# Kernel optimization log

Hardware: AMD Instinct MI355X
Metric: run time of the kernel (lower is better)

## Reference

```python
import jax, jax.numpy as jnp
import numpy as np

N = 100000          # number of active sparse points
GRID = 800          # coordinate grid extent (2D)
KS = 9              # 3x3 kernel offsets
C_IN = 24
C_HID = 144         # round(24 * 6)
C_OUT = 24
EPS = 1e-5


def _build_kernel_map():
    """Build MinkowskiEngine-style kernel map for a 3x3 stride-1 channelwise conv.
    Returns (in_idx, out_idx, off_id), each [KS*N] int32. Invalid (no neighbor)
    entries point to sentinel row N so the padded gather/scatter is a no-op."""
    rng = np.random.default_rng(0)
    flat = rng.choice(GRID * GRID, size=N, replace=False)  # unique 2D coords
    ys, xs = flat // GRID, flat % GRID
    coord_to_idx = -np.ones(GRID * GRID, dtype=np.int64)
    coord_to_idx[flat] = np.arange(N)
    in_chunks, out_chunks, off_chunks = [], [], []
    pts = np.arange(N, dtype=np.int64)
    k = 0
    for dy in (-1, 0, 1):
        for dx in (-1, 0, 1):
            ny, nx = ys + dy, xs + dx
            inside = (ny >= 0) & (ny < GRID) & (nx >= 0) & (nx < GRID)
            nflat = np.clip(ny, 0, GRID - 1) * GRID + np.clip(nx, 0, GRID - 1)
            nidx = np.where(inside, coord_to_idx[nflat], -1)
            valid = nidx >= 0
            in_chunks.append(np.where(valid, nidx, N))
            out_chunks.append(np.where(valid, pts, N))
            off_chunks.append(np.full(N, k, dtype=np.int64))
            k += 1
    in_idx = np.concatenate(in_chunks).astype(np.int32)
    out_idx = np.concatenate(out_chunks).astype(np.int32)
    off_id = np.concatenate(off_chunks).astype(np.int32)
    return in_idx, out_idx, off_id


def setup_inputs() -> dict:
    key = jax.random.key(0)
    ks = jax.random.split(key, 4)
    in_idx, out_idx, off_id = _build_kernel_map()
    return {
        "feats": jax.random.normal(ks[0], (N, C_IN), jnp.float32),
        "w1": jax.random.normal(ks[1], (C_IN, C_HID), jnp.float32) * 0.1,
        "g1": jnp.ones((C_HID,), jnp.float32),
        "b1": jnp.zeros((C_HID,), jnp.float32),
        "w2": jax.random.normal(ks[2], (KS, C_HID), jnp.float32) * 0.1,
        "g2": jnp.ones((C_HID,), jnp.float32),
        "b2": jnp.zeros((C_HID,), jnp.float32),
        "w3": jax.random.normal(ks[3], (C_HID, C_OUT), jnp.float32) * 0.1,
        "g3": jnp.ones((C_OUT,), jnp.float32),
        "b3": jnp.zeros((C_OUT,), jnp.float32),
        "in_idx": jnp.asarray(in_idx),
        "out_idx": jnp.asarray(out_idx),
        "off_id": jnp.asarray(off_id),
    }


def _bn(x, g, b):
    # MinkowskiBatchNorm forward (training mode): per-channel stats over points
    m = jnp.mean(x, axis=0)
    v = jnp.var(x, axis=0)
    return (x - m) * jax.lax.rsqrt(v + EPS) * g + b


def _relu6(x):
    return jnp.clip(x, 0.0, 6.0)


def _channelwise_conv3x3(x, w2, in_idx, out_idx, off_id):
    # gather-multiply-scatter: out[p, c] = sum_k w2[k, c] * x[nbr_k(p), c]
    xp = jnp.concatenate([x, jnp.zeros((1, x.shape[1]), x.dtype)], axis=0)  # sentinel row
    contrib = xp[in_idx] * w2[off_id]                     # [KS*N, C_HID]
    out = jnp.zeros((N + 1, x.shape[1]), x.dtype).at[out_idx].add(contrib)
    return out[:N]


def reference(feats, w1, g1, b1, w2, g2, b2, w3, g3, b3, in_idx, out_idx, off_id):
    x = _relu6(_bn(feats @ w1, g1, b1))                   # 1x1 expand
    x = _relu6(_bn(_channelwise_conv3x3(x, w2, in_idx, out_idx, off_id), g2, b2))
    x = _bn(x @ w3, g3, b3)                               # 1x1 project
    return x + feats                                      # residual (in==out, stride==1)
```

## Files before the change

### kernel.cpp

```cpp
#include <hip/hip_runtime.h>

#define N_PTS 100000
#define KSZ 9
#define C_IN 24
#define C_HID 144
#define C_OUT 24
#define G4_HID 36
#define G4_OUT 6
#define EPSV 1e-5f

#define X1N_OFF   0
#define X1N_SIZE  ((N_PTS + 1) * C_HID)
#define X2_OFF    (X1N_OFF + X1N_SIZE)
#define X2_SIZE   (N_PTS * C_HID)
#define ST_OFF    (X2_OFF + X2_SIZE)
#define MU1_O     (ST_OFF + 0)
#define M1_O      (ST_OFF + 32)
#define SC1_O     (ST_OFF + 640)
#define SH1_O     (ST_OFF + 800)
#define SUM2_O    (ST_OFF + 960)
#define SQ2_O     (ST_OFF + 1120)
#define SC2_O     (ST_OFF + 1280)
#define SH2_O     (ST_OFF + 1440)
#define SUM3_O    (ST_OFF + 1600)
#define SQ3_O     (ST_OFF + 1632)
#define SC3_O     (ST_OFF + 1664)
#define SH3_O     (ST_OFF + 1696)
#define ST_SIZE   1728
#define Y3_OFF    0

__device__ inline float4 f4z() { return make_float4(0.f, 0.f, 0.f, 0.f); }
__device__ inline float4 f4_add(float4 a, float4 b) {
    return make_float4(a.x + b.x, a.y + b.y, a.z + b.z, a.w + b.w);
}
__device__ inline float4 f4_fma4(float4 a, float4 b, float4 c) {
    return make_float4(fmaf(a.x, b.x, c.x), fmaf(a.y, b.y, c.y),
                       fmaf(a.z, b.z, c.z), fmaf(a.w, b.w, c.w));
}
__device__ inline float4 f4_fma_s(float s, float4 b, float4 c) {
    return make_float4(fmaf(s, b.x, c.x), fmaf(s, b.y, c.y),
                       fmaf(s, b.z, c.z), fmaf(s, b.w, c.w));
}
__device__ inline float4 f4_clamp6(float4 a) {
    return make_float4(fminf(fmaxf(a.x, 0.f), 6.f), fminf(fmaxf(a.y, 0.f), 6.f),
                       fminf(fmaxf(a.z, 0.f), 6.f), fminf(fmaxf(a.w, 0.f), 6.f));
}
__device__ inline float f4_get(const float4& v, int e) {
    return e == 0 ? v.x : (e == 1 ? v.y : (e == 2 ? v.z : v.w));
}

__global__ void k_init(float* ws) {
    int t = threadIdx.x;
    for (int i = t; i < ST_SIZE; i += 256) ws[ST_OFF + i] = 0.f;
    if (t < C_HID) ws[X1N_OFF + (size_t)N_PTS * C_HID + t] = 0.f;
}

#define MROWS 128
__device__ inline float task_acc(const float* tile, int cnt, int task) {
    if (task < 576) {
        int i = task / 24, j = task % 24;
        float a = 0.f;
        for (int r = 0; r < cnt; r++) a += tile[r * 24 + i] * tile[r * 24 + j];
        return a;
    }
    int k = task - 576;
    float a = 0.f;
    for (int r = 0; r < cnt; r++) a += tile[r * 24 + k];
    return a;
}
__global__ void k_moments(const float* __restrict__ feats, float* __restrict__ ws) {
    __shared__ float tile[MROWS * C_IN];
    int t = threadIdx.x;
    float acc0 = 0.f, acc1 = 0.f, acc2 = 0.f;
    int nChunks = (N_PTS + MROWS - 1) / MROWS;
    for (int ch = blockIdx.x; ch < nChunks; ch += gridDim.x) {
        int r0 = ch * MROWS;
        int cnt = min(MROWS, N_PTS - r0);
        __syncthreads();
        for (int e = t; e < cnt * C_IN; e += 256) tile[e] = feats[(size_t)r0 * C_IN + e];
        __syncthreads();
        acc0 += task_acc(tile, cnt, t);
        acc1 += task_acc(tile, cnt, t + 256);
        if (t < 88) acc2 += task_acc(tile, cnt, t + 512);
    }
    {
        int task = t;
        atomicAdd(&ws[M1_O + task], acc0);
    }
    {
        int task = t + 256;
        atomicAdd(&ws[M1_O + task], acc1);
    }
    if (t < 88) {
        int task = t + 512;
        if (task < 576) atomicAdd(&ws[M1_O + task], acc2);
        else            atomicAdd(&ws[MU1_O + task - 576], acc2);
    }
}

__global__ void k_fin1(const float* __restrict__ w1, const float* __restrict__ g1,
                       const float* __restrict__ b1, float* __restrict__ ws) {
    int c = threadIdx.x;
    if (c >= C_HID) return;
    float wc[C_IN];
    for (int k = 0; k < C_IN; k++) wc[k] = w1[k * C_HID + c];
    const float invN = 1.f / (float)N_PTS;
    float mean = 0.f;
    for (int k = 0; k < C_IN; k++) mean += ws[MU1_O + k] * wc[k];
    mean *= invN;
    float e2 = 0.f;
    for (int i = 0; i < C_IN; i++) {
        float s = 0.f;
        for (int j = 0; j < C_IN; j++) s += ws[M1_O + i * 24 + j] * wc[j];
        e2 += wc[i] * s;
    }
    e2 *= invN;
    float var = e2 - mean * mean;
    float s1 = g1[c] * rsqrtf(var + EPSV);
    ws[SC1_O + c] = s1;
    ws[SH1_O + c] = b1[c] - mean * s1;
}

__global__ void k_gemm1(const float* __restrict__ feats, const float* __restrict__ w1,
                        float* __restrict__ ws) {
    __shared__ float4 w1s[C_IN * G4_HID];
    __shared__ float4 sc[G4_HID], sh[G4_HID];
    int t = threadIdx.x;
    const float4* w1v = (const float4*)w1;
    for (int e = t; e < C_IN * G4_HID; e += 256) w1s[e] = w1v[e];
    if (t < G4_HID) {
        sc[t] = ((const float4*)(ws + SC1_O))[t];
        sh[t] = ((const float4*)(ws + SH1_O))[t];
    }
    __syncthreads();
    float4* x1v = (float4*)(ws + X1N_OFF);
    const int T = N_PTS * G4_HID;
    for (int tau = blockIdx.x * 256 + t; tau < T; tau += gridDim.x * 256) {
        int p = tau / G4_HID;
        int g = tau % G4_HID;
        const float4* fr = (const float4*)(feats + (size_t)p * C_IN);
        float4 acc = f4z();
#pragma unroll
        for (int q = 0; q < 6; q++) {
            float4 fq = fr[q];
            acc = f4_fma_s(fq.x, w1s[(4 * q + 0) * G4_HID + g], acc);
            acc = f4_fma_s(fq.y, w1s[(4 * q + 1) * G4_HID + g], acc);
            acc = f4_fma_s(fq.z, w1s[(4 * q + 2) * G4_HID + g], acc);
            acc = f4_fma_s(fq.w, w1s[(4 * q + 3) * G4_HID + g], acc);
        }
        x1v[tau] = f4_clamp6(f4_fma4(acc, sc[g], sh[g]));
    }
}

__global__ void k_conv(const float* __restrict__ w2, const int* __restrict__ in_idx,
                       float* __restrict__ ws) {
    __shared__ float4 w2s[KSZ * G4_HID];
    __shared__ float lsum[C_HID], lsq[C_HID];
    int t = threadIdx.x;
    for (int e = t; e < KSZ * G4_HID; e += 256) w2s[e] = ((const float4*)w2)[e];
    if (t < C_HID) { lsum[t] = 0.f; lsq[t] = 0.f; }
    __syncthreads();
    const float4* x1v = (const float4*)(ws + X1N_OFF);
    float4* x2v = (float4*)(ws + X2_OFF);
    bool active = t < 252;
    int pt = t / 36, g = t % 36;
    float4 rs = f4z(), rq = f4z();
    int nChunks = (N_PTS + 6) / 7;
    for (int ch = blockIdx.x; ch < nChunks; ch += gridDim.x) {
        int p = ch * 7 + pt;
        if (active && p < N_PTS) {
            int idxs[KSZ];
#pragma unroll
            for (int k = 0; k < KSZ; k++) idxs[k] = in_idx[k * N_PTS + p];
            float4 acc = f4z();
#pragma unroll
            for (int k = 0; k < KSZ; k++) {
                float4 v = x1v[(size_t)idxs[k] * G4_HID + g];
                acc = f4_fma4(w2s[k * G4_HID + g], v, acc);
            }
            x2v[(size_t)p * G4_HID + g] = acc;
            rs = f4_add(rs, acc);
            rq = f4_fma4(acc, acc, rq);
        }
    }
    if (active) {
        atomicAdd(&lsum[4 * g + 0], rs.x); atomicAdd(&lsum[4 * g + 1], rs.y);
        atomicAdd(&lsum[4 * g + 2], rs.z); atomicAdd(&lsum[4 * g + 3], rs.w);
        atomicAdd(&lsq[4 * g + 0], rq.x);  atomicAdd(&lsq[4 * g + 1], rq.y);
        atomicAdd(&lsq[4 * g + 2], rq.z);  atomicAdd(&lsq[4 * g + 3], rq.w);
    }
    __syncthreads();
    if (t < C_HID) {
        atomicAdd(&ws[SUM2_O + t], lsum[t]);
        atomicAdd(&ws[SQ2_O + t], lsq[t]);
    }
}

__global__ void k_fin2(const float* __restrict__ g2, const float* __restrict__ b2,
                       float* __restrict__ ws) {
    int c = threadIdx.x;
    if (c >= C_HID) return;
    const float invN = 1.f / (float)N_PTS;
    float mean = ws[SUM2_O + c] * invN;
    float var = ws[SQ2_O + c] * invN - mean * mean;
    float s = g2[c] * rsqrtf(var + EPSV);
    ws[SC2_O + c] = s;
    ws[SH2_O + c] = b2[c] - mean * s;
}

__global__ void k_gemm2(const float* __restrict__ w3, float* __restrict__ ws) {
    __shared__ float4 w3s[C_HID * G4_OUT];
    __shared__ float4 sc2[G4_HID], sh2[G4_HID];
    int t = threadIdx.x;
    for (int e = t; e < C_HID * G4_OUT; e += 256) w3s[e] = ((const float4*)w3)[e];
    if (t < G4_HID) {
        sc2[t] = ((const float4*)(ws + SC2_O))[t];
        sh2[t] = ((const float4*)(ws + SH2_O))[t];
    }
    __syncthreads();
    const float4* x2v = (const float4*)(ws + X2_OFF);
    float4* y3v = (float4*)(ws + Y3_OFF);
    int gtid = blockIdx.x * 256 + t;
    int r0 = gtid * 2, r1 = r0 + 1;
    bool v0 = r0 < N_PTS, v1 = r1 < N_PTS;
    float4 a0[G4_OUT], a1[G4_OUT];
#pragma unroll
    for (int c4 = 0; c4 < G4_OUT; c4++) { a0[c4] = f4z(); a1[c4] = f4z(); }
    for (int h4 = 0; h4 < G4_HID; h4++) {
        float4 xa = v0 ? x2v[(size_t)r0 * G4_HID + h4] : f4z();
        float4 xb = v1 ? x2v[(size_t)r1 * G4_HID + h4] : f4z();
        float4 s = sc2[h4], b = sh2[h4];
        xa = f4_clamp6(f4_fma4(xa, s, b));
        xb = f4_clamp6(f4_fma4(xb, s, b));
#pragma unroll
        for (int e = 0; e < 4; e++) {
            int h = h4 * 4 + e;
            float fa = f4_get(xa, e), fb = f4_get(xb, e);
#pragma unroll
            for (int c4 = 0; c4 < G4_OUT; c4++) {
                float4 w = w3s[h * G4_OUT + c4];
                a0[c4] = f4_fma_s(fa, w, a0[c4]);
                a1[c4] = f4_fma_s(fb, w, a1[c4]);
            }
        }
    }
    if (v0) {
#pragma unroll
        for (int c4 = 0; c4 < G4_OUT; c4++) y3v[(size_t)r0 * G4_OUT + c4] = a0[c4];
    }
    if (v1) {
#pragma unroll
        for (int c4 = 0; c4 < G4_OUT; c4++) y3v[(size_t)r1 * G4_OUT + c4] = a1[c4];
    }
}

__global__ void k_red3(float* __restrict__ ws) {
    int t = threadIdx.x;
    const float* y3 = ws + Y3_OFF;
    float rs = 0.f, rq = 0.f;
    const int total = N_PTS * C_OUT;
    for (int e = blockIdx.x * 192 + t; e < total; e += gridDim.x * 192) {
        float v = y3[e];
        rs += v; rq += v * v;
    }
    __shared__ float ls[192], lq[192];
    ls[t] = rs; lq[t] = rq;
    __syncthreads();
    if (t < C_OUT) {
        float s = 0.f, q = 0.f;
        for (int u = t; u < 192; u += C_OUT) { s += ls[u]; q += lq[u]; }
        atomicAdd(&ws[SUM3_O + t], s);
        atomicAdd(&ws[SQ3_O + t], q);
    }
}

__global__ void k_fin3(const float* __restrict__ g3, const float* __restrict__ b3,
                       float* __restrict__ ws) {
    int c = threadIdx.x;
    if (c >= C_OUT) return;
    const float invN = 1.f / (float)N_PTS;
    float mean = ws[SUM3_O + c] * invN;
    float var = ws[SQ3_O + c] * invN - mean * mean;
    float s = g3[c] * rsqrtf(var + EPSV);
    ws[SC3_O + c] = s;
    ws[SH3_O + c] = b3[c] - mean * s;
}

__global__ void k_out(const float* __restrict__ feats, const float* __restrict__ ws,
                      float* __restrict__ out) {
    int t4 = blockIdx.x * 256 + threadIdx.x;
    const int T = N_PTS * G4_OUT;
    if (t4 >= T) return;
    int g = t4 % G4_OUT;
    float4 y = ((const float4*)(ws + Y3_OFF))[t4];
    float4 s = ((const float4*)(ws + SC3_O))[g];
    float4 b = ((const float4*)(ws + SH3_O))[g];
    float4 f = ((const float4*)feats)[t4];
    ((float4*)out)[t4] = f4_add(f4_fma4(y, s, b), f);
}

extern "C" void kernel_launch(void* const* d_in, const int* in_sizes, int n_in,
                              void* d_out, int out_size, void* d_ws, size_t ws_size,
                              hipStream_t stream) {
    const float* feats = (const float*)d_in[0];
    const float* w1 = (const float*)d_in[1];
    const float* g1 = (const float*)d_in[2];
    const float* b1 = (const float*)d_in[3];
    const float* w2 = (const float*)d_in[4];
    const float* g2 = (const float*)d_in[5];
    const float* b2 = (const float*)d_in[6];
    const float* w3 = (const float*)d_in[7];
    const float* g3 = (const float*)d_in[8];
    const float* b3 = (const float*)d_in[9];
    const int* in_idx = (const int*)d_in[10];
    float* ws = (float*)d_ws;
    float* out = (float*)d_out;

    hipLaunchKernelGGL(k_init, dim3(1), dim3(256), 0, stream, ws);
    hipLaunchKernelGGL(k_moments, dim3(256), dim3(256), 0, stream, feats, ws);
    hipLaunchKernelGGL(k_fin1, dim3(1), dim3(192), 0, stream, w1, g1, b1, ws);
    hipLaunchKernelGGL(k_gemm1, dim3(2048), dim3(256), 0, stream, feats, w1, ws);
    hipLaunchKernelGGL(k_conv, dim3(2048), dim3(256), 0, stream, w2, in_idx, ws);
    hipLaunchKernelGGL(k_fin2, dim3(1), dim3(192), 0, stream, g2, b2, ws);
    hipLaunchKernelGGL(k_gemm2, dim3((N_PTS + 511) / 512), dim3(256), 0, stream, w3, ws);
    hipLaunchKernelGGL(k_red3, dim3(512), dim3(192), 0, stream, ws);
    hipLaunchKernelGGL(k_fin3, dim3(1), dim3(64), 0, stream, g3, b3, ws);
    hipLaunchKernelGGL(k_out, dim3((N_PTS * G4_OUT + 255) / 256), dim3(256), 0, stream,
                       feats, ws, out);
}
```

Baseline: 278.6 us.

## Store hidden activations in fp16 and fuse BN3 stats into tiled gemm2

The expanded activations x1 and the conv output x2 are now stored as packed half2 values, which halves the memory traffic of the gather-heavy conv and of the gemm2 read. Conv weights are held in registers instead of shared memory, and each thread handles 8 channels. gemm2 is rewritten to stage a 64-point tile in shared memory and to reduce the BN3 sum and sum-of-squares with wave shuffles, which removes the separate k_red3 pass. Rounding to fp16 before the batch norms can cost accuracy.

```diff
diff --git a/kernel.cpp b/kernel.cpp
--- a/kernel.cpp
+++ b/kernel.cpp
@@ -1,4 +1,5 @@
 #include <hip/hip_runtime.h>
+#include <hip/hip_fp16.h>
 
 #define N_PTS 100000
 #define KSZ 9
@@ -6,28 +7,27 @@
 #define C_HID 144
 #define C_OUT 24
 #define G4_HID 36
+#define G8_HID 18
 #define G4_OUT 6
 #define EPSV 1e-5f
 
-#define X1N_OFF   0
-#define X1N_SIZE  ((N_PTS + 1) * C_HID)
-#define X2_OFF    (X1N_OFF + X1N_SIZE)
-#define X2_SIZE   (N_PTS * C_HID)
-#define ST_OFF    (X2_OFF + X2_SIZE)
-#define MU1_O     (ST_OFF + 0)
-#define M1_O      (ST_OFF + 32)
-#define SC1_O     (ST_OFF + 640)
-#define SH1_O     (ST_OFF + 800)
-#define SUM2_O    (ST_OFF + 960)
-#define SQ2_O     (ST_OFF + 1120)
-#define SC2_O     (ST_OFF + 1280)
-#define SH2_O     (ST_OFF + 1440)
-#define SUM3_O    (ST_OFF + 1600)
-#define SQ3_O     (ST_OFF + 1632)
-#define SC3_O     (ST_OFF + 1664)
-#define SH3_O     (ST_OFF + 1696)
+#define X1H_B     0
+#define X2H_B     28800288
+#define Y3F_O     14400072
+#define ST_O      16800072
+#define MU1_O     (ST_O + 0)
+#define M1_O      (ST_O + 32)
+#define SC1_O     (ST_O + 640)
+#define SH1_O     (ST_O + 800)
+#define SUM2_O    (ST_O + 960)
+#define SQ2_O     (ST_O + 1120)
+#define SC2_O     (ST_O + 1280)
+#define SH2_O     (ST_O + 1440)
+#define SUM3_O    (ST_O + 1600)
+#define SQ3_O     (ST_O + 1632)
+#define SC3_O     (ST_O + 1664)
+#define SH3_O     (ST_O + 1696)
 #define ST_SIZE   1728
-#define Y3_OFF    0
 
 __device__ inline float4 f4z() { return make_float4(0.f, 0.f, 0.f, 0.f); }
 __device__ inline float4 f4_add(float4 a, float4 b) {
@@ -45,14 +45,22 @@
     return make_float4(fminf(fmaxf(a.x, 0.f), 6.f), fminf(fmaxf(a.y, 0.f), 6.f),
                        fminf(fmaxf(a.z, 0.f), 6.f), fminf(fmaxf(a.w, 0.f), 6.f));
 }
-__device__ inline float f4_get(const float4& v, int e) {
-    return e == 0 ? v.x : (e == 1 ? v.y : (e == 2 ? v.z : v.w));
-}
-
-__global__ void k_init(float* ws) {
-    int t = threadIdx.x;
-    for (int i = t; i < ST_SIZE; i += 256) ws[ST_OFF + i] = 0.f;
-    if (t < C_HID) ws[X1N_OFF + (size_t)N_PTS * C_HID + t] = 0.f;
+__device__ inline unsigned pack2(float a, float b) {
+    __half2 h = __floats2half2_rn(a, b);
+    return *reinterpret_cast<unsigned*>(&h);
+}
+__device__ inline float2 uph(unsigned u) {
+    __half2 h = *reinterpret_cast<__half2*>(&u);
+    return __half22float2(h);
+}
+
+__global__ __launch_bounds__(256) void k_init(float* ws) {
+    int t = threadIdx.x;
+    for (int i = t; i < ST_SIZE; i += 256) ws[ST_O + i] = 0.f;
+    if (t < G8_HID) {
+        uint4 z; z.x = 0u; z.y = 0u; z.z = 0u; z.w = 0u;
+        ((uint4*)ws)[(size_t)N_PTS * G8_HID + t] = z;
+    }
 }
 
 #define MROWS 128
@@ -68,7 +76,8 @@
     for (int r = 0; r < cnt; r++) a += tile[r * 24 + k];
     return a;
 }
-__global__ void k_moments(const float* __restrict__ feats, float* __restrict__ ws) {
+__global__ __launch_bounds__(256) void k_moments(const float* __restrict__ feats,
+                                                 float* __restrict__ ws) {
     __shared__ float tile[MROWS * C_IN];
     int t = threadIdx.x;
     float acc0 = 0.f, acc1 = 0.f, acc2 = 0.f;
@@ -83,14 +92,8 @@
         acc1 += task_acc(tile, cnt, t + 256);
         if (t < 88) acc2 += task_acc(tile, cnt, t + 512);
     }
-    {
-        int task = t;
-        atomicAdd(&ws[M1_O + task], acc0);
-    }
-    {
-        int task = t + 256;
-        atomicAdd(&ws[M1_O + task], acc1);
-    }
+    atomicAdd(&ws[M1_O + t], acc0);
+    atomicAdd(&ws[M1_O + t + 256], acc1);
     if (t < 88) {
         int task = t + 512;
         if (task < 576) atomicAdd(&ws[M1_O + task], acc2);
@@ -121,73 +124,98 @@
     ws[SH1_O + c] = b1[c] - mean * s1;
 }
 
-__global__ void k_gemm1(const float* __restrict__ feats, const float* __restrict__ w1,
-                        float* __restrict__ ws) {
+__global__ __launch_bounds__(256) void k_gemm1(const float* __restrict__ feats,
+                                               const float* __restrict__ w1,
+                                               float* __restrict__ ws) {
     __shared__ float4 w1s[C_IN * G4_HID];
     __shared__ float4 sc[G4_HID], sh[G4_HID];
     int t = threadIdx.x;
-    const float4* w1v = (const float4*)w1;
-    for (int e = t; e < C_IN * G4_HID; e += 256) w1s[e] = w1v[e];
+    for (int e = t; e < C_IN * G4_HID; e += 256) w1s[e] = ((const float4*)w1)[e];
     if (t < G4_HID) {
         sc[t] = ((const float4*)(ws + SC1_O))[t];
         sh[t] = ((const float4*)(ws + SH1_O))[t];
     }
     __syncthreads();
-    float4* x1v = (float4*)(ws + X1N_OFF);
-    const int T = N_PTS * G4_HID;
+    uint4* x1u = (uint4*)ws;
+    const int T = N_PTS * G8_HID;
     for (int tau = blockIdx.x * 256 + t; tau < T; tau += gridDim.x * 256) {
-        int p = tau / G4_HID;
-        int g = tau % G4_HID;
+        int p = tau / G8_HID;
+        int g = tau % G8_HID;
         const float4* fr = (const float4*)(feats + (size_t)p * C_IN);
-        float4 acc = f4z();
+        float4 a0 = f4z(), a1 = f4z();
 #pragma unroll
         for (int q = 0; q < 6; q++) {
             float4 fq = fr[q];
-            acc = f4_fma_s(fq.x, w1s[(4 * q + 0) * G4_HID + g], acc);
-            acc = f4_fma_s(fq.y, w1s[(4 * q + 1) * G4_HID + g], acc);
-            acc = f4_fma_s(fq.z, w1s[(4 * q + 2) * G4_HID + g], acc);
-            acc = f4_fma_s(fq.w, w1s[(4 * q + 3) * G4_HID + g], acc);
-        }
-        x1v[tau] = f4_clamp6(f4_fma4(acc, sc[g], sh[g]));
-    }
-}
-
-__global__ void k_conv(const float* __restrict__ w2, const int* __restrict__ in_idx,
-                       float* __restrict__ ws) {
-    __shared__ float4 w2s[KSZ * G4_HID];
+            a0 = f4_fma_s(fq.x, w1s[(4 * q + 0) * G4_HID + 2 * g], a0);
+            a1 = f4_fma_s(fq.x, w1s[(4 * q + 0) * G4_HID + 2 * g + 1], a1);
+            a0 = f4_fma_s(fq.y, w1s[(4 * q + 1) * G4_HID + 2 * g], a0);
+            a1 = f4_fma_s(fq.y, w1s[(4 * q + 1) * G4_HID + 2 * g + 1], a1);
+            a0 = f4_fma_s(fq.z, w1s[(4 * q + 2) * G4_HID + 2 * g], a0);
+            a1 = f4_fma_s(fq.z, w1s[(4 * q + 2) * G4_HID + 2 * g + 1], a1);
+            a0 = f4_fma_s(fq.w, w1s[(4 * q + 3) * G4_HID + 2 * g], a0);
+            a1 = f4_fma_s(fq.w, w1s[(4 * q + 3) * G4_HID + 2 * g + 1], a1);
+        }
+        a0 = f4_clamp6(f4_fma4(a0, sc[2 * g], sh[2 * g]));
+        a1 = f4_clamp6(f4_fma4(a1, sc[2 * g + 1], sh[2 * g + 1]));
+        uint4 o;
+        o.x = pack2(a0.x, a0.y); o.y = pack2(a0.z, a0.w);
+        o.z = pack2(a1.x, a1.y); o.w = pack2(a1.z, a1.w);
+        x1u[tau] = o;
+    }
+}
+
+__global__ __launch_bounds__(256) void k_conv(const float* __restrict__ w2,
+                                              const int* __restrict__ in_idx,
+                                              float* __restrict__ ws) {
     __shared__ float lsum[C_HID], lsq[C_HID];
     int t = threadIdx.x;
-    for (int e = t; e < KSZ * G4_HID; e += 256) w2s[e] = ((const float4*)w2)[e];
     if (t < C_HID) { lsum[t] = 0.f; lsq[t] = 0.f; }
     __syncthreads();
-    const float4* x1v = (const float4*)(ws + X1N_OFF);
-    float4* x2v = (float4*)(ws + X2_OFF);
+    const uint4* x1u = (const uint4*)ws;
+    uint4* x2u = (uint4*)((char*)ws + X2H_B);
     bool active = t < 252;
-    int pt = t / 36, g = t % 36;
-    float4 rs = f4z(), rq = f4z();
-    int nChunks = (N_PTS + 6) / 7;
+    int pt = t / G8_HID, g = t % G8_HID;
+    const float4* w2v = (const float4*)w2;
+    float4 wA[KSZ], wB[KSZ];
+#pragma unroll
+    for (int k = 0; k < KSZ; k++) {
+        wA[k] = w2v[k * G4_HID + 2 * g];
+        wB[k] = w2v[k * G4_HID + 2 * g + 1];
+    }
+    float4 rsA = f4z(), rsB = f4z(), rqA = f4z(), rqB = f4z();
+    int nChunks = (N_PTS + 13) / 14;
     for (int ch = blockIdx.x; ch < nChunks; ch += gridDim.x) {
-        int p = ch * 7 + pt;
+        int p = ch * 14 + pt;
         if (active && p < N_PTS) {
-            int idxs[KSZ];
-#pragma unroll
-            for (int k = 0; k < KSZ; k++) idxs[k] = in_idx[k * N_PTS + p];
-            float4 acc = f4z();
+            int idx[KSZ];
+#pragma unroll
+            for (int k = 0; k < KSZ; k++) idx[k] = in_idx[k * N_PTS + p];
+            float4 aA = f4z(), aB = f4z();
 #pragma unroll
             for (int k = 0; k < KSZ; k++) {
-                float4 v = x1v[(size_t)idxs[k] * G4_HID + g];
-                acc = f4_fma4(w2s[k * G4_HID + g], v, acc);
+                uint4 v = x1u[(size_t)idx[k] * G8_HID + g];
+                float2 f0 = uph(v.x), f1 = uph(v.y), f2 = uph(v.z), f3 = uph(v.w);
+                aA = f4_fma4(wA[k], make_float4(f0.x, f0.y, f1.x, f1.y), aA);
+                aB = f4_fma4(wB[k], make_float4(f2.x, f2.y, f3.x, f3.y), aB);
             }
-            x2v[(size_t)p * G4_HID + g] = acc;
-            rs = f4_add(rs, acc);
-            rq = f4_fma4(acc, acc, rq);
+            uint4 o;
+            o.x = pack2(aA.x, aA.y); o.y = pack2(aA.z, aA.w);
+            o.z = pack2(aB.x, aB.y); o.w = pack2(aB.z, aB.w);
+            x2u[(size_t)p * G8_HID + g] = o;
+            rsA = f4_add(rsA, aA); rsB = f4_add(rsB, aB);
+            rqA = f4_fma4(aA, aA, rqA); rqB = f4_fma4(aB, aB, rqB);
         }
     }
     if (active) {
-        atomicAdd(&lsum[4 * g + 0], rs.x); atomicAdd(&lsum[4 * g + 1], rs.y);
-        atomicAdd(&lsum[4 * g + 2], rs.z); atomicAdd(&lsum[4 * g + 3], rs.w);
-        atomicAdd(&lsq[4 * g + 0], rq.x);  atomicAdd(&lsq[4 * g + 1], rq.y);
-        atomicAdd(&lsq[4 * g + 2], rq.z);  atomicAdd(&lsq[4 * g + 3], rq.w);
+        int c0 = 8 * g;
+        atomicAdd(&lsum[c0 + 0], rsA.x); atomicAdd(&lsum[c0 + 1], rsA.y);
+        atomicAdd(&lsum[c0 + 2], rsA.z); atomicAdd(&lsum[c0 + 3], rsA.w);
+        atomicAdd(&lsum[c0 + 4], rsB.x); atomicAdd(&lsum[c0 + 5], rsB.y);
+        atomicAdd(&lsum[c0 + 6], rsB.z); atomicAdd(&lsum[c0 + 7], rsB.w);
+        atomicAdd(&lsq[c0 + 0], rqA.x);  atomicAdd(&lsq[c0 + 1], rqA.y);
+        atomicAdd(&lsq[c0 + 2], rqA.z);  atomicAdd(&lsq[c0 + 3], rqA.w);
+        atomicAdd(&lsq[c0 + 4], rqB.x);  atomicAdd(&lsq[c0 + 5], rqB.y);
+        atomicAdd(&lsq[c0 + 6], rqB.z);  atomicAdd(&lsq[c0 + 7], rqB.w);
     }
     __syncthreads();
     if (t < C_HID) {
@@ -208,69 +236,84 @@
     ws[SH2_O + c] = b2[c] - mean * s;
 }
 
-__global__ void k_gemm2(const float* __restrict__ w3, float* __restrict__ ws) {
-    __shared__ float4 w3s[C_HID * G4_OUT];
-    __shared__ float4 sc2[G4_HID], sh2[G4_HID];
-    int t = threadIdx.x;
-    for (int e = t; e < C_HID * G4_OUT; e += 256) w3s[e] = ((const float4*)w3)[e];
-    if (t < G4_HID) {
-        sc2[t] = ((const float4*)(ws + SC2_O))[t];
-        sh2[t] = ((const float4*)(ws + SH2_O))[t];
-    }
-    __syncthreads();
-    const float4* x2v = (const float4*)(ws + X2_OFF);
-    float4* y3v = (float4*)(ws + Y3_OFF);
-    int gtid = blockIdx.x * 256 + t;
-    int r0 = gtid * 2, r1 = r0 + 1;
-    bool v0 = r0 < N_PTS, v1 = r1 < N_PTS;
-    float4 a0[G4_OUT], a1[G4_OUT];
-#pragma unroll
-    for (int c4 = 0; c4 < G4_OUT; c4++) { a0[c4] = f4z(); a1[c4] = f4z(); }
-    for (int h4 = 0; h4 < G4_HID; h4++) {
-        float4 xa = v0 ? x2v[(size_t)r0 * G4_HID + h4] : f4z();
-        float4 xb = v1 ? x2v[(size_t)r1 * G4_HID + h4] : f4z();
-        float4 s = sc2[h4], b = sh2[h4];
-        xa = f4_clamp6(f4_fma4(xa, s, b));
-        xb = f4_clamp6(f4_fma4(xb, s, b));
-#pragma unroll
-        for (int e = 0; e < 4; e++) {
-            int h = h4 * 4 + e;
-            float fa = f4_get(xa, e), fb = f4_get(xb, e);
-#pragma unroll
-            for (int c4 = 0; c4 < G4_OUT; c4++) {
-                float4 w = w3s[h * G4_OUT + c4];
-                a0[c4] = f4_fma_s(fa, w, a0[c4]);
-                a1[c4] = f4_fma_s(fb, w, a1[c4]);
-            }
-        }
-    }
-    if (v0) {
-#pragma unroll
-        for (int c4 = 0; c4 < G4_OUT; c4++) y3v[(size_t)r0 * G4_OUT + c4] = a0[c4];
-    }
-    if (v1) {
-#pragma unroll
-        for (int c4 = 0; c4 < G4_OUT; c4++) y3v[(size_t)r1 * G4_OUT + c4] = a1[c4];
-    }
-}
-
-__global__ void k_red3(float* __restrict__ ws) {
-    int t = threadIdx.x;
-    const float* y3 = ws + Y3_OFF;
-    float rs = 0.f, rq = 0.f;
-    const int total = N_PTS * C_OUT;
-    for (int e = blockIdx.x * 192 + t; e < total; e += gridDim.x * 192) {
-        float v = y3[e];
-        rs += v; rq += v * v;
-    }
-    __shared__ float ls[192], lq[192];
-    ls[t] = rs; lq[t] = rq;
+#define TP 64
+__global__ __launch_bounds__(256) void k_gemm2(const float* __restrict__ w3,
+                                               float* __restrict__ ws) {
+    __shared__ float xs[TP * 145];
+    __shared__ float w3s[C_HID * C_OUT];
+    __shared__ float sc2s[C_HID], sh2s[C_HID];
+    __shared__ float ssum[C_OUT], ssq[C_OUT];
+    int t = threadIdx.x;
+    for (int e = t; e < C_HID * C_OUT / 4; e += 256)
+        ((float4*)w3s)[e] = ((const float4*)w3)[e];
+    if (t < C_HID) { sc2s[t] = ws[SC2_O + t]; sh2s[t] = ws[SH2_O + t]; }
+    if (t < C_OUT) { ssum[t] = 0.f; ssq[t] = 0.f; }
+    __syncthreads();
+    const uint4* x2u = (const uint4*)((char*)ws + X2H_B);
+    int p0 = blockIdx.x * TP;
+    for (int e = t; e < TP * G8_HID; e += 256) {
+        int row = e / G8_HID, col = e % G8_HID;
+        int p = p0 + row;
+        int c0 = 8 * col;
+        float v[8];
+        if (p < N_PTS) {
+            uint4 u = x2u[(size_t)p * G8_HID + col];
+            float2 f0 = uph(u.x), f1 = uph(u.y), f2 = uph(u.z), f3 = uph(u.w);
+            v[0] = f0.x; v[1] = f0.y; v[2] = f1.x; v[3] = f1.y;
+            v[4] = f2.x; v[5] = f2.y; v[6] = f3.x; v[7] = f3.y;
+#pragma unroll
+            for (int i = 0; i < 8; i++)
+                v[i] = fminf(fmaxf(fmaf(v[i], sc2s[c0 + i], sh2s[c0 + i]), 0.f), 6.f);
+        } else {
+#pragma unroll
+            for (int i = 0; i < 8; i++) v[i] = 0.f;
+        }
+#pragma unroll
+        for (int i = 0; i < 8; i++) xs[row * 145 + c0 + i] = v[i];
+    }
+    __syncthreads();
+    int pl = t & 63, cg = t >> 6;
+    int c0 = 6 * cg;
+    float acc[6] = {0.f, 0.f, 0.f, 0.f, 0.f, 0.f};
+    const float* xr = xs + pl * 145;
+#pragma unroll 4
+    for (int h = 0; h < C_HID; h++) {
+        float x = xr[h];
+#pragma unroll
+        for (int j = 0; j < 6; j++) acc[j] = fmaf(x, w3s[h * C_OUT + c0 + j], acc[j]);
+    }
+    int p = p0 + pl;
+    bool valid = p < N_PTS;
+    float* y3 = ws + Y3F_O;
+    if (valid) {
+#pragma unroll
+        for (int j = 0; j < 6; j++) y3[(size_t)p * C_OUT + c0 + j] = acc[j];
+    }
+    float s[6], q[6];
+#pragma unroll
+    for (int j = 0; j < 6; j++) {
+        s[j] = valid ? acc[j] : 0.f;
+        q[j] = s[j] * s[j];
+    }
+#pragma unroll
+    for (int off = 32; off > 0; off >>= 1) {
+#pragma unroll
+        for (int j = 0; j < 6; j++) {
+            s[j] += __shfl_down(s[j], off);
+            q[j] += __shfl_down(q[j], off);
+        }
+    }
+    if (pl == 0) {
+#pragma unroll
+        for (int j = 0; j < 6; j++) {
+            atomicAdd(&ssum[c0 + j], s[j]);
+            atomicAdd(&ssq[c0 + j], q[j]);
+        }
+    }
     __syncthreads();
     if (t < C_OUT) {
-        float s = 0.f, q = 0.f;
-        for (int u = t; u < 192; u += C_OUT) { s += ls[u]; q += lq[u]; }
-        atomicAdd(&ws[SUM3_O + t], s);
-        atomicAdd(&ws[SQ3_O + t], q);
+        atomicAdd(&ws[SUM3_O + t], ssum[t]);
+        atomicAdd(&ws[SQ3_O + t], ssq[t]);
     }
 }
 
@@ -286,13 +329,14 @@
     ws[SH3_O + c] = b3[c] - mean * s;
 }
 
-__global__ void k_out(const float* __restrict__ feats, const float* __restrict__ ws,
-                      float* __restrict__ out) {
+__global__ __launch_bounds__(256) void k_out(const float* __restrict__ feats,
+                                             const float* __restrict__ ws,
+                                             float* __restrict__ out) {
     int t4 = blockIdx.x * 256 + threadIdx.x;
     const int T = N_PTS * G4_OUT;
     if (t4 >= T) return;
     int g = t4 % G4_OUT;
-    float4 y = ((const float4*)(ws + Y3_OFF))[t4];
+    float4 y = ((const float4*)(ws + Y3F_O))[t4];
     float4 s = ((const float4*)(ws + SC3_O))[g];
     float4 b = ((const float4*)(ws + SH3_O))[g];
     float4 f = ((const float4*)feats)[t4];
@@ -322,8 +366,7 @@
     hipLaunchKernelGGL(k_gemm1, dim3(2048), dim3(256), 0, stream, feats, w1, ws);
     hipLaunchKernelGGL(k_conv, dim3(2048), dim3(256), 0, stream, w2, in_idx, ws);
     hipLaunchKernelGGL(k_fin2, dim3(1), dim3(192), 0, stream, g2, b2, ws);
-    hipLaunchKernelGGL(k_gemm2, dim3((N_PTS + 511) / 512), dim3(256), 0, stream, w3, ws);
-    hipLaunchKernelGGL(k_red3, dim3(512), dim3(192), 0, stream, ws);
+    hipLaunchKernelGGL(k_gemm2, dim3((N_PTS + TP - 1) / TP), dim3(256), 0, stream, w3, ws);
     hipLaunchKernelGGL(k_fin3, dim3(1), dim3(64), 0, stream, g3, b3, ws);
     hipLaunchKernelGGL(k_out, dim3((N_PTS * G4_OUT + 255) / 256), dim3(256), 0, stream,
                        feats, ws, out);
```

Measured after the change: 319.9 us. 14.8% more time.
